# Kernel tuning notes

Measured on AMD Instinct MI355X. Metric: run time of the kernel, lower is better.

The kernel has to match this reference:

```python
import jax, jax.numpy as jnp
import numpy as np

B, C, N = 16, 4, 100
S = 96            # args.seq_len
L = 2 * S         # time-domain length
F = S + 1         # rfft bins == module's self.seq_len
D = 128           # d_model
M = 16            # delay components
H = 8             # num_heads (hard-coded)
HD = D // H       # head_dim
P = S             # pred_len


def clin(x, wr, wi, br, bi):
    # complex Linear: y = x @ W^T + b
    w = jax.lax.complex(wr, wi)
    b = jax.lax.complex(br, bi)
    return x @ w.T + b


def crelu(z):
    return jax.lax.complex(jax.nn.relu(z.real), jax.nn.relu(z.imag))


def mha(q, kv, wq, bq, wk, bk, wv, bv, wo, bo):
    # q: [B,C,N,D], kv: [B,C,N,M,D]
    Bq, Cq, Nq, Dq = q.shape
    Mq = kv.shape[3]
    Q = (q @ wq.T + bq).reshape(Bq, Cq, Nq, H, HD).transpose(0, 1, 3, 2, 4)          # [B,C,H,N,HD]
    K = (kv @ wk.T + bk).reshape(Bq, Cq, Nq, Mq, H, HD).transpose(0, 1, 4, 2, 3, 5)  # [B,C,H,N,M,HD]
    V = (kv @ wv.T + bv).reshape(Bq, Cq, Nq, Mq, H, HD).transpose(0, 1, 4, 2, 3, 5)
    K = K.reshape(Bq, Cq, H, Nq * Mq, HD)
    V = V.reshape(Bq, Cq, H, Nq * Mq, HD)
    scale = float(D) ** -0.5
    scores = jnp.einsum('bchne,bchme->bchnm', Q, K) * scale   # [B,C,H,N,N*M]
    w = jax.nn.softmax(scores, axis=-1)
    o = jnp.einsum('bchnm,bchme->bchne', w, V)                # [B,C,H,N,HD]
    o = o.transpose(0, 1, 3, 2, 4).reshape(Bq, Cq, Nq, Dq)
    return o @ wo.T + bo


def setup_inputs() -> dict:
    key = jax.random.key(0)
    ks = jax.random.split(key, 48)
    i = iter(range(48))
    def n(shape, s=0.05):
        return jax.random.normal(ks[next(i)], shape, jnp.float32) * s
    inp = {}
    inp['xp'] = jax.random.normal(ks[next(i)], (B, C, N, L), jnp.float32)
    inp['freq_weights'] = jnp.ones((F,), jnp.float32)
    inp['temp_real'] = n((M, F), 0.02)
    inp['temp_imag'] = n((M, F), 0.02)
    # complex Linears (real/imag weight & bias)
    inp['fc1_wr'] = n((D, F)); inp['fc1_wi'] = n((D, F)); inp['fc1_br'] = jnp.zeros((D,), jnp.float32); inp['fc1_bi'] = jnp.zeros((D,), jnp.float32)
    inp['fc2_wr'] = n((D, D)); inp['fc2_wi'] = n((D, D)); inp['fc2_br'] = jnp.zeros((D,), jnp.float32); inp['fc2_bi'] = jnp.zeros((D,), jnp.float32)
    inp['fc3_wr'] = n((F, D)); inp['fc3_wi'] = n((F, D)); inp['fc3_br'] = jnp.zeros((F,), jnp.float32); inp['fc3_bi'] = jnp.zeros((F,), jnp.float32)
    inp['fc4_wr'] = n((D, F)); inp['fc4_wi'] = n((D, F)); inp['fc4_br'] = jnp.zeros((D,), jnp.float32); inp['fc4_bi'] = jnp.zeros((D,), jnp.float32)
    inp['fc5_wr'] = n((D, D)); inp['fc5_wi'] = n((D, D)); inp['fc5_br'] = jnp.zeros((D,), jnp.float32); inp['fc5_bi'] = jnp.zeros((D,), jnp.float32)
    for pfx in ('ra', 'ia'):
        for nm in ('wq', 'wk', 'wv', 'wo'):
            inp[f'{pfx}_{nm}'] = n((D, D))
            inp[f'{pfx}_b{nm[1]}'] = n((D,), 0.01)
    inp['op1_w'] = n((4 * P, 2 * P)); inp['op1_b'] = jnp.zeros((4 * P,), jnp.float32)
    inp['op2_w'] = n((P, 4 * P)); inp['op2_b'] = jnp.zeros((P,), jnp.float32)
    return inp


def reference(xp, freq_weights, temp_real, temp_imag,
              fc1_wr, fc1_wi, fc1_br, fc1_bi,
              fc2_wr, fc2_wi, fc2_br, fc2_bi,
              fc3_wr, fc3_wi, fc3_br, fc3_bi,
              fc4_wr, fc4_wi, fc4_br, fc4_bi,
              fc5_wr, fc5_wi, fc5_br, fc5_bi,
              ra_wq, ra_bq, ra_wk, ra_bk, ra_wv, ra_bv, ra_wo, ra_bo,
              ia_wq, ia_bq, ia_wk, ia_bk, ia_wv, ia_bv, ia_wo, ia_bo,
              op1_w, op1_b, op2_w, op2_b):
    xf = jnp.fft.rfft(xp, axis=-1)                       # [B,C,N,F] complex64
    xf = xf * jax.nn.sigmoid(freq_weights)
    temp = jax.lax.complex(temp_real, temp_imag)          # [M,F]
    xt = xf[..., None, :] * temp                          # [B,C,N,M,F]
    e = crelu(clin(xt, fc1_wr, fc1_wi, fc1_br, fc1_bi))
    e = clin(e, fc2_wr, fc2_wi, fc2_br, fc2_bi)           # [B,C,N,M,D]
    g = crelu(clin(xf, fc4_wr, fc4_wi, fc4_br, fc4_bi))
    g = clin(g, fc5_wr, fc5_wi, fc5_br, fc5_bi)           # [B,C,N,D]
    o_r = mha(g.real, e.real, ra_wq, ra_bq, ra_wk, ra_bk, ra_wv, ra_bv, ra_wo, ra_bo) + g.real
    o_i = mha(g.imag, e.imag, ia_wq, ia_bq, ia_wk, ia_bk, ia_wv, ia_bv, ia_wo, ia_bo) + g.imag
    o = jax.lax.complex(o_r, o_i)
    o = clin(o, fc3_wr, fc3_wi, fc3_br, fc3_bi)           # [B,C,N,F]
    ot = jnp.fft.irfft(o, n=L, axis=-1)                   # [B,C,N,L] float32
    of = ot.reshape(-1, 2 * P)
    h = jax.nn.relu(of @ op1_w.T + op1_b)
    out = (h @ op2_w.T + op2_b).reshape(B, C, N, P)
    return out
```

## Files before the change

kernel.cpp:

```cpp
#include <hip/hip_runtime.h>
#include <hip/hip_bf16.h>

#define NB 16
#define NC 4
#define NN 100
#define NL 192
#define NF 97
#define ND 128
#define NM 16
#define NH 8
#define NHD 16
#define NP 96
#define NR (NB*NC*NN)
#define NBC (NB*NC)
#define KP1 224

typedef __bf16 bf16x8 __attribute__((ext_vector_type(8)));
typedef float f32x4 __attribute__((ext_vector_type(4)));
typedef float f32x16 __attribute__((ext_vector_type(16)));
typedef short s16x8 __attribute__((ext_vector_type(8)));
typedef short s16x4 __attribute__((ext_vector_type(4)));
typedef float f32x4v __attribute__((ext_vector_type(4)));

__device__ __forceinline__ float bf2f(unsigned short u){
  union { unsigned int i; float f; } x; x.i = ((unsigned int)u) << 16; return x.f;
}
__device__ __forceinline__ unsigned short f2bf(float v){
  __hip_bfloat16 h = __float2bfloat16(v);
  return *reinterpret_cast<unsigned short*>(&h);
}
__device__ __forceinline__ float fexp2(float x){
  float r; asm("v_exp_f32 %0, %1\n\ts_nop 0" : "=v"(r) : "v"(x)); return r;
}

__global__ void k_prep(const float* __restrict__ fw,
                       const float* __restrict__ fc1_wr, const float* __restrict__ fc1_wi,
                       const float* __restrict__ tr_, const float* __restrict__ ti_,
                       const float* __restrict__ fc4_wr, const float* __restrict__ fc4_wi,
                       const float* __restrict__ op1_w, const float* __restrict__ op2_w,
                       const float* __restrict__ xp,
                       unsigned short* __restrict__ Tt, unsigned short* __restrict__ Wbig,
                       unsigned short* __restrict__ Wg1,
                       unsigned short* __restrict__ Wop1, unsigned short* __restrict__ Wop2,
                       unsigned short* __restrict__ Xpb, unsigned short* __restrict__ Xpbf){
  int b = blockIdx.x, c = threadIdx.x;
  if (b < 256){
    if (c >= KP1) return;
    int l = b;
    float v = 0.f;
    if (l < NL && c < 2*NF){
      int f = (c < NF) ? c : c - NF;
      float s = 1.f/(1.f+expf(-fw[f]));
      int ph = (f*l) % NL;
      float ang = (float)ph * (6.283185307179586f/(float)NL);
      float sv, cv; sincosf(ang, &sv, &cv);
      v = (c < NF) ? s*cv : -s*sv;
    }
    Tt[(size_t)l*KP1 + c] = f2bf(v);
  } else if (b < 256+4096){
    if (c >= KP1) return;
    int nIdx = b - 256;
    int m = nIdx >> 8, p = (nIdx >> 7) & 1, d = nIdx & 127;
    float v = 0.f;
    if (c < 2*NF){
      int f = (c < NF) ? c : c - NF;
      float tr = tr_[m*NF+f], ti = ti_[m*NF+f];
      float wr_ = fc1_wr[d*NF+f], wi_ = fc1_wi[d*NF+f];
      float w1r = tr*wr_ - ti*wi_;
      float w1i = tr*wi_ + ti*wr_;
      if (p == 0) v = (c < NF) ? w1r : -w1i;
      else        v = (c < NF) ? w1i :  w1r;
    }
    Wbig[(size_t)nIdx*KP1 + c] = f2bf(v);
  } else if (b < 256+4096+256){
    if (c >= KP1) return;
    int n = b - (256+4096);
    int p = n >> 7, d = n & 127;
    float v = 0.f;
    if (c < NF) v = p ? fc4_wi[d*NF+c] : fc4_wr[d*NF+c];
    else if (c < 2*NF){
      int f = c - NF;
      v = p ? fc4_wr[d*NF+f] : -fc4_wi[d*NF+f];
    }
    Wg1[(size_t)n*KP1 + c] = f2bf(v);
  } else if (b < 4608+480){
    int i = (b-4608)*256 + c;
    const int N1 = 384*NL;
    if (i < N1){ Wop1[i] = f2bf(op1_w[i]); return; }
    int j = i - N1;
    if (j < 128*384){
      int n = j / 384, t2 = j - n*384;
      Wop2[j] = f2bf((n < NP) ? op2_w[n*384 + t2] : 0.f);
    }
  } else {
    size_t i = ((size_t)(b-5088)*256 + c)*8;
    f32x4v a = *(const f32x4v*)(xp + i);
    f32x4v bb = *(const f32x4v*)(xp + i + 4);
    s16x8 o;
#pragma unroll
    for (int e=0;e<4;e++){ o[e] = (short)f2bf(a[e]); o[4+e] = (short)f2bf(bb[e]); }
    *(s16x8*)(Xpb + i) = o;
    int row = (int)(i / NL);
    int colg = (int)(i % NL) >> 3;
    int rb = row >> 4, rl = row & 15;
    int ch = colg >> 2, cg = colg & 3;
    int lane = rl + (cg << 4);
    *(s16x8*)(Xpbf + ((((size_t)rb*6 + ch)*64 + lane)*8)) = o;
  }
}

__global__ void k_prep2(const float* __restrict__ fc2_wr, const float* __restrict__ fc2_wi,
                        const float* __restrict__ fc2_br, const float* __restrict__ fc2_bi,
                        const float* __restrict__ ra_wk, const float* __restrict__ ra_bk,
                        const float* __restrict__ ra_wv, const float* __restrict__ ra_bv,
                        const float* __restrict__ ia_wk, const float* __restrict__ ia_bk,
                        const float* __restrict__ ia_wv, const float* __restrict__ ia_bv,
                        const float* __restrict__ fc5_wr, const float* __restrict__ fc5_wi,
                        const float* __restrict__ fc5_br, const float* __restrict__ fc5_bi,
                        const float* __restrict__ ra_wq, const float* __restrict__ ra_bq,
                        const float* __restrict__ ia_wq, const float* __restrict__ ia_bq,
                        const float* __restrict__ fc3_wr, const float* __restrict__ fc3_wi,
                        const float* __restrict__ fc3_br, const float* __restrict__ fc3_bi,
                        unsigned short* __restrict__ comb2f, float* __restrict__ cbias,
                        unsigned short* __restrict__ Wg2, float* __restrict__ bg2,
                        float* __restrict__ A_, float* __restrict__ B_, float* __restrict__ c0_){
  __shared__ float icL[NF], isL[NF];
  int b = blockIdx.x, t = threadIdx.x;
  if (b < 1032){
    if (t >= 128) return;
    int k = b >> 3, c = b & 7, d = t;
    if (k == ND){
      if (c >= 4) return;
      const float* w = ra_wk; const float* bb = ra_bk; const float* fb = fc2_br;
      switch(c){
        case 0: w=ra_wk; bb=ra_bk; fb=fc2_br; break;
        case 1: w=ra_wv; bb=ra_bv; fb=fc2_br; break;
        case 2: w=ia_wk; bb=ia_bk; fb=fc2_bi; break;
        case 3: w=ia_wv; bb=ia_bv; fb=fc2_bi; break;
      }
      float s = bb[d];
      for (int j=0;j<ND;j++) s += w[d*ND+j]*fb[j];
      cbias[c*ND+d] = s;
      return;
    }
    const float* w = ra_wk; const float* f2 = fc2_wr; float sign = 1.f;
    switch(c){
      case 0: w=ra_wk; f2=fc2_wr; sign= 1.f; break;
      case 1: w=ra_wk; f2=fc2_wi; sign=-1.f; break;
      case 2: w=ra_wv; f2=fc2_wr; sign= 1.f; break;
      case 3: w=ra_wv; f2=fc2_wi; sign=-1.f; break;
      case 4: w=ia_wk; f2=fc2_wi; sign= 1.f; break;
      case 5: w=ia_wk; f2=fc2_wr; sign= 1.f; break;
      case 6: w=ia_wv; f2=fc2_wi; sign= 1.f; break;
      case 7: w=ia_wv; f2=fc2_wr; sign= 1.f; break;
    }
    float s = 0.f;
    for (int j=0;j<ND;j++) s += w[d*ND+j]*f2[j*ND+k];
    int cOut = c >> 1, p = c & 1;
    int jj = d >> 4, rl = d & 15;
    int col = p*ND + k;
    int ch = col >> 5, cg = (col >> 3) & 3, e = col & 7;
    int lane = rl + (cg << 4);
    comb2f[((((size_t)(cOut*8 + ch))*8 + jj)*64 + lane)*8 + e] = f2bf(sign*s);
  } else if (b < 1032+512){
    int q = b - 1032, c = t;
    int k = c & 127; bool ti = (c >= 128);
    const float SCL = 0.08838834764831845f * 1.4426950408889634f;
    float v = 0.f;
    if (q < 128){
      const float* f5 = ti ? fc5_wi : fc5_wr; float sg = ti ? -1.f : 1.f;
      float s = 0.f;
      for (int j=0;j<ND;j++) s += ra_wq[q*ND+j]*f5[j*ND+k];
      v = sg*s*SCL;
    } else if (q < 256){
      int qq = q-128;
      const float* f5 = ti ? fc5_wr : fc5_wi;
      float s = 0.f;
      for (int j=0;j<ND;j++) s += ia_wq[qq*ND+j]*f5[j*ND+k];
      v = s*SCL;
    } else if (q < 384){
      int d = q-256;
      v = ti ? -fc5_wi[d*ND+k] : fc5_wr[d*ND+k];
    } else {
      int d = q-384;
      v = ti ? fc5_wr[d*ND+k] : fc5_wi[d*ND+k];
    }
    Wg2[(size_t)q*256 + c] = f2bf(v);
    if (c == 0){
      float bb;
      if (q < 128){ bb = ra_bq[q]; for (int j=0;j<ND;j++) bb += ra_wq[q*ND+j]*fc5_br[j]; bb *= SCL; }
      else if (q < 256){ int qq=q-128; bb = ia_bq[qq]; for (int j=0;j<ND;j++) bb += ia_wq[qq*ND+j]*fc5_bi[j]; bb *= SCL; }
      else if (q < 384) bb = fc5_br[q-256];
      else bb = fc5_bi[q-384];
      bg2[q] = bb;
    }
  } else {
    int l = b - 1544, d = t;
    if (d < NF){
      float w = ((d==0)||(d==NF-1)) ? 1.f : 2.f;
      w *= (1.f/(float)NL);
      int ph = (d*l) % NL;
      float ang = (float)ph * (6.283185307179586f/(float)NL);
      float sv, cv; sincosf(ang, &sv, &cv);
      icL[d] = w*cv; isL[d] = w*sv;
    }
    __syncthreads();
    if (d < 128){
      float a = 0.f, bb = 0.f;
      for (int f=0;f<NF;f++){
        float ic = icL[f], is = isL[f];
        float wr = fc3_wr[f*ND+d], wi = fc3_wi[f*ND+d];
        a += ic*wr - is*wi;
        bb -= ic*wi + is*wr;
      }
      A_[l*ND+d] = a; B_[l*ND+d] = bb;
      if (d == 0){
        float cc = 0.f;
        for (int f=0;f<NF;f++) cc += icL[f]*fc3_br[f] - isL[f]*fc3_bi[f];
        c0_[l] = cc;
      }
    }
  }
}

__global__ void k_wt1(const float* __restrict__ A_, const float* __restrict__ B_,
                      const float* __restrict__ c0_,
                      const float* __restrict__ ra_wo, const float* __restrict__ ra_bo,
                      const float* __restrict__ ia_wo, const float* __restrict__ ia_bo,
                      unsigned short* __restrict__ WT1, float* __restrict__ bT1){
  int l = blockIdx.x;
  int c = threadIdx.x;
  float v = 0.f;
  if (l < NL){
    if (c < 128) v = A_[l*ND+c];
    else if (c < 256) v = B_[l*ND+(c-128)];
    else if (c < 384){
      int k = c-256; float s = 0.f;
      for (int j=0;j<ND;j++) s += A_[l*ND+j]*ra_wo[j*ND+k];
      v = s;
    } else {
      int k = c-384; float s = 0.f;
      for (int j=0;j<ND;j++) s += B_[l*ND+j]*ia_wo[j*ND+k];
      v = s;
    }
  }
  WT1[(size_t)l*512 + c] = f2bf(v);
  if (c == 0){
    float bb = 0.f;
    if (l < NL){
      bb = c0_[l];
      for (int j=0;j<ND;j++) bb += A_[l*ND+j]*ra_bo[j] + B_[l*ND+j]*ia_bo[j];
    }
    bT1[l] = bb;
  }
}

template<int MT, int KT, int MODE>
__global__ __launch_bounds__(256) void k_gemm(
    const unsigned short* __restrict__ A, int lda,
    const unsigned short* __restrict__ Bw,
    const float* __restrict__ b0, const float* __restrict__ b1,
    void* __restrict__ Cv, int ldc)
{
  constexpr int NI = MT/32;
  __shared__ unsigned short As[MT][40];
  __shared__ unsigned short Bs[128][40];
  int t = threadIdx.x;
  int bm = blockIdx.x, bn = blockIdx.y;
  int w = t >> 6, l = t & 63;
  int wm = w >> 1, wn = w & 1;
  f32x4 acc[NI][4] = {};
  int r0 = t >> 2, c0 = (t & 3) * 8;
  const unsigned short* Ag = A + (size_t)(bm*MT)*lda;
  const unsigned short* Bg = Bw + (size_t)(bn*128)*KT;
  int lr = l & 15, lk = (l >> 4) * 8;
  for (int k0 = 0; k0 < KT; k0 += 32){
    s16x8 a0 = *(const s16x8*)(Ag + (size_t)r0*lda + k0 + c0);
    s16x8 a1;
    if constexpr (MT == 128) a1 = *(const s16x8*)(Ag + (size_t)(r0+64)*lda + k0 + c0);
    s16x8 bv0 = *(const s16x8*)(Bg + (size_t)r0*KT + k0 + c0);
    s16x8 bv1 = *(const s16x8*)(Bg + (size_t)(r0+64)*KT + k0 + c0);
    __syncthreads();
    *(s16x8*)(&As[r0][c0]) = a0;
    if constexpr (MT == 128) *(s16x8*)(&As[r0+64][c0]) = a1;
    *(s16x8*)(&Bs[r0][c0]) = bv0;
    *(s16x8*)(&Bs[r0+64][c0]) = bv1;
    __syncthreads();
    bf16x8 af[NI], bfr[4];
#pragma unroll
    for (int i=0;i<NI;i++) af[i]  = *(const bf16x8*)(&As[wm*(MT/2) + i*16 + lr][lk]);
#pragma unroll
    for (int j=0;j<4;j++) bfr[j] = *(const bf16x8*)(&Bs[wn*64 + j*16 + lr][lk]);
#pragma unroll
    for (int i=0;i<NI;i++)
#pragma unroll
      for (int j=0;j<4;j++)
        acc[i][j] = __builtin_amdgcn_mfma_f32_16x16x32_bf16(af[i], bfr[j], acc[i][j], 0, 0, 0);
  }
  int lr4 = (l >> 4) * 4, lc = l & 15;
#pragma unroll
  for (int i=0;i<NI;i++){
#pragma unroll
    for (int j=0;j<4;j++){
      int n = bn*128 + wn*64 + j*16 + lc;
      float bias;
      if constexpr (MODE == 1) bias = ((n>>7)&1) ? b1[n&127] : b0[n&127];
      else if constexpr (MODE == 4) bias = (n < NP) ? b0[n] : 0.f;
      else if constexpr (MODE == 6 || MODE == 7) bias = 0.f;
      else bias = b0[n];
#pragma unroll
      for (int q=0;q<4;q++){
        int row = bm*MT + wm*(MT/2) + i*16 + lr4 + q;
        float v = acc[i][j][q] + bias;
        if constexpr (MODE == 1 || MODE == 3) v = fmaxf(v, 0.f);
        if constexpr (MODE == 4){
          if (n < NP) ((float*)Cv)[(size_t)row*ldc + n] = v;
        } else if constexpr (MODE == 6){
          if (n < NL) ((unsigned short*)Cv)[(size_t)row*ldc + n] = f2bf(v);
        } else if constexpr (MODE == 7){
          if (n < NL){
            int m2 = row >> 8, rt = row & 255;
            int jj = rt >> 4, rl2 = rt & 15;
            int ch = n >> 5, cg = (n >> 3) & 3, e = n & 7;
            int lane = rl2 + (cg << 4);
            ((unsigned short*)Cv)[((((size_t)(m2*6 + ch))*16 + jj)*64 + lane)*8 + e] = f2bf(v);
          }
        } else {
          ((unsigned short*)Cv)[(size_t)row*ldc + n] = f2bf(v);
        }
      }
    }
  }
}

__global__ __launch_bounds__(256, 4) void k_fuse(
    const unsigned short* __restrict__ Xpbf,
    const unsigned short* __restrict__ Wbig2f,
    const float* __restrict__ fc1_br, const float* __restrict__ fc1_bi,
    const unsigned short* __restrict__ comb2f,
    const float* __restrict__ cbias,
    unsigned short* __restrict__ Kg,
    unsigned short* __restrict__ Vt)
{
  __shared__ unsigned short act2f[8][4][64][8];
  int t = threadIdx.x;
  int bm = blockIdx.x, m = blockIdx.y;
  int w = t >> 6, l = t & 63;
  int lc = l & 15, lr4 = (l >> 4) * 4;
  int rbase = bm*64;

  f32x4 acc1[4][4] = {};
  const unsigned short* Af = Xpbf + ((size_t)(bm*4)*6)*512;
  const unsigned short* Bf = Wbig2f + ((size_t)m*6)*16*512;
#pragma unroll 2
  for (int ch = 0; ch < 6; ch++){
    bf16x8 af[4], bfj[4];
#pragma unroll
    for (int i=0;i<4;i++)
      af[i] = *(const bf16x8*)(Af + ((size_t)i*6 + ch)*512 + l*8);
#pragma unroll
    for (int j=0;j<4;j++)
      bfj[j] = *(const bf16x8*)(Bf + ((size_t)ch*16 + w*4 + j)*512 + l*8);
#pragma unroll
    for (int i=0;i<4;i++)
#pragma unroll
      for (int j=0;j<4;j++)
        acc1[i][j] = __builtin_amdgcn_mfma_f32_16x16x32_bf16(af[i], bfj[j], acc1[i][j], 0, 0, 0);
  }
#pragma unroll
  for (int i=0;i<4;i++){
#pragma unroll
    for (int j=0;j<4;j++){
      int col = w*64 + j*16 + lc;
      float bias = ((col>>7)&1) ? fc1_bi[col&127] : fc1_br[col&127];
      int ch = col >> 5, cg = (col >> 3) & 3, e = col & 7;
#pragma unroll
      for (int q=0;q<4;q++)
        act2f[ch][i][(lr4 + q) + (cg << 4)][e] = f2bf(fmaxf(acc1[i][j][q] + bias, 0.f));
    }
  }
  __syncthreads();

  for (int bn2 = 0; bn2 < 4; bn2++){
    const unsigned short* Cf = comb2f + ((size_t)bn2*8)*8*512;
    int call = bn2 >> 1, isV = bn2 & 1;
    if (!isV){
      f32x4 accS[2][4] = {};
#pragma unroll 4
      for (int ch = 0; ch < 8; ch++){
        bf16x8 af[4], bfr[2];
#pragma unroll
        for (int i=0;i<4;i++)
          af[i] = *(const bf16x8*)(&act2f[ch][i][l][0]);
#pragma unroll
        for (int j=0;j<2;j++)
          bfr[j] = *(const bf16x8*)(Cf + ((size_t)ch*8 + w*2 + j)*512 + l*8);
#pragma unroll
        for (int j=0;j<2;j++)
#pragma unroll
          for (int i=0;i<4;i++)
            accS[j][i] = __builtin_amdgcn_mfma_f32_16x16x32_bf16(bfr[j], af[i], accS[j][i], 0, 0, 0);
      }
#pragma unroll
      for (int j=0;j<2;j++){
        int n2q = w*32 + j*16 + lr4;
        f32x4v cb4 = *(const f32x4v*)(cbias + bn2*128 + n2q);
        int h = n2q >> 4, d0 = n2q & 15;
#pragma unroll
        for (int i=0;i<4;i++){
          int rr = rbase + i*16 + lc;
          int bc = rr/100, n = rr - bc*100;
          int kk = m*100 + n;
          s16x4 v4;
#pragma unroll
          for (int q=0;q<4;q++) v4[q] = (short)f2bf(accS[j][i][q] + cb4[q]);
          *(s16x4*)(Kg + ((((size_t)(call*NBC + bc))*8 + h)*1600 + kk)*16 + d0) = v4;
        }
      }
    } else {
      f32x4 acc[4][2] = {};
#pragma unroll 4
      for (int ch = 0; ch < 8; ch++){
        bf16x8 af[4], bfr[2];
#pragma unroll
        for (int i=0;i<4;i++)
          af[i] = *(const bf16x8*)(&act2f[ch][i][l][0]);
#pragma unroll
        for (int j=0;j<2;j++)
          bfr[j] = *(const bf16x8*)(Cf + ((size_t)ch*8 + w*2 + j)*512 + l*8);
#pragma unroll
        for (int i=0;i<4;i++)
#pragma unroll
          for (int j=0;j<2;j++)
            acc[i][j] = __builtin_amdgcn_mfma_f32_16x16x32_bf16(af[i], bfr[j], acc[i][j], 0, 0, 0);
      }
#pragma unroll
      for (int i=0;i<4;i++){
        int rr0 = rbase + i*16 + lr4;
        int bc = rr0/100, n = rr0 - bc*100;
        int kk = m*100 + n;
#pragma unroll
        for (int j=0;j<2;j++){
          int n2 = w*32 + j*16 + lc;
          float bias = cbias[bn2*128 + n2];
          s16x4 v4;
#pragma unroll
          for (int q=0;q<4;q++) v4[q] = (short)f2bf(acc[i][j][q] + bias);
          *(s16x4*)(Vt + ((size_t)(call*NBC + bc)*128 + n2)*1600 + kk) = v4;
        }
      }
    }
  }
}

__global__ __launch_bounds__(256, 4) void k_attn3(
    const unsigned short* __restrict__ BIG,
    const unsigned short* __restrict__ Kg,
    const unsigned short* __restrict__ Vt,
    unsigned short* __restrict__ BIGo)
{
  int h = blockIdx.x, bc = blockIdx.y, call = blockIdx.z;
  int t = threadIdx.x;
  int wv = t >> 6, l = t & 63;
  int lane31 = l & 31, hi = l >> 5;
  int qoff = call*128, ooff = 512 + call*128;
  __shared__ float xch[4][32];

  const unsigned short* Kh = Kg + (((size_t)(call*NBC + bc))*8 + h)*1600*16;
  const unsigned short* Vh = Vt + ((((size_t)(call*NBC + bc))*8 + h)*16)*1600;

  int qrow = wv*32 + lane31;
  bf16x8 qf = {};
  if (qrow < NN)
    qf = *(const bf16x8*)(BIG + (size_t)(bc*NN + qrow)*768 + qoff + h*NHD + hi*8);

  f32x16 acc = {};
  float m = -1e30f, lsum = 0.f;
  const f32x16 zero16 = {};
  int vd = lane31 & 15;

  auto tile = [&](bf16x8 kf0, bf16x8 kf1, int cc0){
    bf16x8 vfr[4];
#pragma unroll
    for (int ks=0; ks<4; ks++)
      vfr[ks] = *(const bf16x8*)(Vh + (size_t)vd*1600 + cc0 + ks*16 + hi*8);

    __builtin_amdgcn_s_setprio(1);
    f32x16 s0 = __builtin_amdgcn_mfma_f32_32x32x16_bf16(kf0, qf, zero16, 0, 0, 0);
    f32x16 s1 = __builtin_amdgcn_mfma_f32_32x32x16_bf16(kf1, qf, zero16, 0, 0, 0);
    __builtin_amdgcn_s_setprio(0);
    float p[32];
#pragma unroll
    for (int r2=0;r2<16;r2++){ p[r2] = s0[r2]; p[16+r2] = s1[r2]; }

    float t8[8];
#pragma unroll
    for (int r2=0;r2<8;r2++)
      t8[r2] = fmaxf(fmaxf(p[r2], p[r2+8]), fmaxf(p[r2+16], p[r2+24]));
#pragma unroll
    for (int r2=0;r2<4;r2++) t8[r2] = fmaxf(t8[r2], t8[r2+4]);
    float pm = fmaxf(fmaxf(t8[0], t8[1]), fmaxf(t8[2], t8[3]));
    pm = fmaxf(pm, __shfl_xor(pm, 32));

    if (__any(pm > m + 8.f)){
      float M = fmaxf(m, pm);
      float alpha = fexp2(m - M);
      lsum *= alpha;
      if (l < 32) xch[wv][l] = alpha;
#pragma unroll
      for (int r2=0;r2<16;r2++)
        acc[r2] *= xch[wv][(r2&3) + 8*(r2>>2) + 4*hi];
      m = M;
    }
#pragma unroll
    for (int r2=0;r2<32;r2++) p[r2] = fexp2(p[r2] - m);
    float s8[8];
#pragma unroll
    for (int r2=0;r2<8;r2++) s8[r2] = (p[r2] + p[r2+8]) + (p[r2+16] + p[r2+24]);
#pragma unroll
    for (int r2=0;r2<4;r2++) s8[r2] += s8[r2+4];
    lsum += (s8[0]+s8[1]) + (s8[2]+s8[3]);

#pragma unroll
    for (int ks=0; ks<4; ks++){
      unsigned int a, b, c, dd, sa, sb, sc2, sd;
      asm("v_cvt_pk_bf16_f32 %0, %1, %2" : "=v"(a)  : "v"(p[8*ks+0]), "v"(p[8*ks+1]));
      asm("v_cvt_pk_bf16_f32 %0, %1, %2" : "=v"(b)  : "v"(p[8*ks+4]), "v"(p[8*ks+5]));
      asm("v_cvt_pk_bf16_f32 %0, %1, %2" : "=v"(c)  : "v"(p[8*ks+2]), "v"(p[8*ks+3]));
      asm("v_cvt_pk_bf16_f32 %0, %1, %2" : "=v"(dd) : "v"(p[8*ks+6]), "v"(p[8*ks+7]));
      sa = __shfl_xor(a, 32); sb = __shfl_xor(b, 32);
      sc2 = __shfl_xor(c, 32); sd = __shfl_xor(dd, 32);
      union { unsigned int u[4]; bf16x8 v; } pu;
      pu.u[0] = hi ? sb : a;
      pu.u[1] = hi ? sd : c;
      pu.u[2] = hi ? b  : sa;
      pu.u[3] = hi ? dd : sc2;
      acc = __builtin_amdgcn_mfma_f32_32x32x16_bf16(pu.v, vfr[ks], acc, 0, 0, 0);
    }
  };

  bf16x8 k0a = *(const bf16x8*)(Kh + (size_t)lane31*16 + hi*8);
  bf16x8 k1a = *(const bf16x8*)(Kh + (size_t)(32 + lane31)*16 + hi*8);
  bf16x8 k0b, k1b;
#pragma unroll 1
  for (int cc0 = 0; cc0 < NN*NM; cc0 += 128){
    if (cc0 + 64 < NN*NM){
      k0b = *(const bf16x8*)(Kh + (size_t)(cc0 + 64 + lane31)*16 + hi*8);
      k1b = *(const bf16x8*)(Kh + (size_t)(cc0 + 96 + lane31)*16 + hi*8);
    }
    tile(k0a, k1a, cc0);
    if (cc0 + 64 >= NN*NM) break;
    if (cc0 + 128 < NN*NM){
      k0a = *(const bf16x8*)(Kh + (size_t)(cc0 + 128 + lane31)*16 + hi*8);
      k1a = *(const bf16x8*)(Kh + (size_t)(cc0 + 160 + lane31)*16 + hi*8);
    }
    tile(k0b, k1b, cc0 + 64);
  }

  lsum += __shfl_xor(lsum, 32);
  float inv = 1.f / lsum;
  if (l < 32) xch[wv][l] = inv;
  if (lane31 < 16){
    int d = lane31;
#pragma unroll
    for (int r2=0;r2<16;r2++){
      int q = (r2&3) + 8*(r2>>2) + 4*hi;
      int qr2 = wv*32 + q;
      if (qr2 < NN){
        float iv = xch[wv][q];
        BIGo[(size_t)(bc*NN + qr2)*768 + ooff + h*NHD + d] = f2bf(acc[r2]*iv);
      }
    }
  }
}

extern "C" void kernel_launch(void* const* d_in, const int* in_sizes, int n_in,
                              void* d_out, int out_size, void* d_ws, size_t ws_size,
                              hipStream_t stream){
  const float* xp     = (const float*)d_in[0];
  const float* fw     = (const float*)d_in[1];
  const float* temp_r = (const float*)d_in[2];
  const float* temp_i = (const float*)d_in[3];
  const float* fc1_wr=(const float*)d_in[4],  *fc1_wi=(const float*)d_in[5],
             *fc1_br=(const float*)d_in[6],  *fc1_bi=(const float*)d_in[7];
  const float* fc2_wr=(const float*)d_in[8],  *fc2_wi=(const float*)d_in[9],
             *fc2_br=(const float*)d_in[10], *fc2_bi=(const float*)d_in[11];
  const float* fc3_wr=(const float*)d_in[12], *fc3_wi=(const float*)d_in[13],
             *fc3_br=(const float*)d_in[14], *fc3_bi=(const float*)d_in[15];
  const float* fc4_wr=(const float*)d_in[16], *fc4_wi=(const float*)d_in[17],
             *fc4_br=(const float*)d_in[18], *fc4_bi=(const float*)d_in[19];
  const float* fc5_wr=(const float*)d_in[20], *fc5_wi=(const float*)d_in[21],
             *fc5_br=(const float*)d_in[22], *fc5_bi=(const float*)d_in[23];
  const float* ra_wq=(const float*)d_in[24], *ra_bq=(const float*)d_in[25],
             *ra_wk=(const float*)d_in[26], *ra_bk=(const float*)d_in[27],
             *ra_wv=(const float*)d_in[28], *ra_bv=(const float*)d_in[29],
             *ra_wo=(const float*)d_in[30], *ra_bo=(const float*)d_in[31];
  const float* ia_wq=(const float*)d_in[32], *ia_bq=(const float*)d_in[33],
             *ia_wk=(const float*)d_in[34], *ia_bk=(const float*)d_in[35],
             *ia_wv=(const float*)d_in[36], *ia_bv=(const float*)d_in[37],
             *ia_wo=(const float*)d_in[38], *ia_bo=(const float*)d_in[39];
  const float* op1_w=(const float*)d_in[40], *op1_b=(const float*)d_in[41],
             *op2_w=(const float*)d_in[42], *op2_b=(const float*)d_in[43];
  float* out = (float*)d_out;

  char* ws = (char*)d_ws;
  size_t off = 0;
  auto alloc = [&](size_t bytes)->char*{
    char* p = ws + off;
    off += (bytes + 255) & ~(size_t)255;
    return p;
  };
  unsigned short* Tt     = (unsigned short*)alloc((size_t)256*KP1*2);
  unsigned short* Wbig   = (unsigned short*)alloc((size_t)4096*KP1*2);
  unsigned short* Wbig2f = (unsigned short*)alloc((size_t)4096*NL*2);
  unsigned short* comb2f = (unsigned short*)alloc((size_t)512*256*2);
  float* cbias= (float*)alloc((size_t)4*ND*4);
  unsigned short* Wg1    = (unsigned short*)alloc((size_t)256*KP1*2);
  unsigned short* Wg1f   = (unsigned short*)alloc((size_t)256*NL*2);
  unsigned short* Wg2    = (unsigned short*)alloc((size_t)512*256*2);
  float* bg2  = (float*)alloc((size_t)512*4);
  float* A_   = (float*)alloc((size_t)NL*ND*4);
  float* B_   = (float*)alloc((size_t)NL*ND*4);
  float* c0_  = (float*)alloc((size_t)NL*4);
  unsigned short* WT1    = (unsigned short*)alloc((size_t)256*512*2);
  float* bT1  = (float*)alloc((size_t)256*4);
  unsigned short* Wop1   = (unsigned short*)alloc((size_t)384*NL*2);
  unsigned short* Wop2   = (unsigned short*)alloc((size_t)128*384*2);
  unsigned short* Xpb    = (unsigned short*)alloc((size_t)NR*NL*2);
  unsigned short* Xpbf   = (unsigned short*)alloc((size_t)NR*NL*2);
  unsigned short* actg   = (unsigned short*)alloc((size_t)NR*256*2);
  unsigned short* Kg     = (unsigned short*)alloc((size_t)2*NBC*NH*1600*16*2);
  unsigned short* Vt     = (unsigned short*)alloc((size_t)2*NBC*NH*16*1600*2);
  unsigned short* BIG    = (unsigned short*)alloc((size_t)NR*768*2);
  unsigned short* C1     = (unsigned short*)alloc((size_t)NR*256*2);
  unsigned short* hbuf   = (unsigned short*)alloc((size_t)NR*384*2);

  k_prep<<<5688, 256, 0, stream>>>(fw, fc1_wr, fc1_wi, temp_r, temp_i,
                                   fc4_wr, fc4_wi, op1_w, op2_w, xp,
                                   Tt, Wbig, Wg1, Wop1, Wop2, Xpb, Xpbf);
  k_prep2<<<1736, 256, 0, stream>>>(fc2_wr, fc2_wi, fc2_br, fc2_bi,
                                    ra_wk, ra_bk, ra_wv, ra_bv,
                                    ia_wk, ia_bk, ia_wv, ia_bv,
                                    fc5_wr, fc5_wi, fc5_br, fc5_bi,
                                    ra_wq, ra_bq, ia_wq, ia_bq,
                                    fc3_wr, fc3_wi, fc3_br, fc3_bi,
                                    comb2f, cbias, Wg2, bg2, A_, B_, c0_);
  k_wt1<<<256, 512, 0, stream>>>(A_, B_, c0_, ra_wo, ra_bo, ia_wo, ia_bo, WT1, bT1);
  k_gemm<128,KP1,7><<<dim3(32, 2), 256, 0, stream>>>(Wbig, KP1, Tt, nullptr, nullptr, Wbig2f, NL);
  k_gemm<128,KP1,6><<<dim3(2, 2), 256, 0, stream>>>(Wg1, KP1, Tt, nullptr, nullptr, Wg1f, NL);

  k_gemm<64,NL,1><<<dim3(100, 2), 256, 0, stream>>>(Xpb, NL, Wg1f, fc4_br, fc4_bi, actg, 256);
  k_gemm<64,256,2><<<dim3(100, 4), 256, 0, stream>>>(actg, 256, Wg2, bg2, nullptr, BIG, 768);
  k_fuse<<<dim3(100, NM), 256, 0, stream>>>(Xpbf, Wbig2f, fc1_br, fc1_bi, comb2f, cbias, Kg, Vt);
  k_attn3<<<dim3(NH, NBC, 2), 256, 0, stream>>>(BIG, Kg, Vt, BIG);
  k_gemm<64,512,2><<<dim3(100, 2), 256, 0, stream>>>(BIG+256, 768, WT1, bT1, nullptr, C1, 256);
  k_gemm<64,192,3><<<dim3(100, 3), 256, 0, stream>>>(C1, 256, Wop1, op1_b, nullptr, hbuf, 384);
  k_gemm<64,384,4><<<dim3(100, 1), 256, 0, stream>>>(hbuf, 384, Wop2, op2_b, nullptr, out, NP);
}
```

Before: 199.3 us.

## Split attention key range in two with a separate log-sum-exp combine kernel

The attention kernel now splits the 1600 keys into two halves across an extra grid dimension, doubling the number of blocks from 1024 to 2048. Each half writes unnormalized fp32 partial outputs plus its running max and sum. A new combine kernel merges the halves and writes bf16 into the big activation buffer. The goal is better CU occupancy on the attention stage, paid for with an extra launch, partial-result traffic, and the loss of the double-buffered K prefetch.

Result: slower. 207.1 us (+4.0%).

```diff
diff --git a/kernel.cpp b/kernel.cpp
--- a/kernel.cpp
+++ b/kernel.cpp
@@ -457,13 +457,15 @@
     const unsigned short* __restrict__ BIG,
     const unsigned short* __restrict__ Kg,
     const unsigned short* __restrict__ Vt,
-    unsigned short* __restrict__ BIGo)
+    float* __restrict__ Opart,
+    float* __restrict__ MLp)
 {
-  int h = blockIdx.x, bc = blockIdx.y, call = blockIdx.z;
+  int h = blockIdx.x, bc = blockIdx.y, z = blockIdx.z;
+  int call = z >> 1, half = z & 1;
   int t = threadIdx.x;
   int wv = t >> 6, l = t & 63;
   int lane31 = l & 31, hi = l >> 5;
-  int qoff = call*128, ooff = 512 + call*128;
+  int qoff = call*128;
   __shared__ float xch[4][32];
 
   const unsigned short* Kh = Kg + (((size_t)(call*NBC + bc))*8 + h)*1600*16;
@@ -479,7 +481,13 @@
   const f32x16 zero16 = {};
   int vd = lane31 & 15;
 
-  auto tile = [&](bf16x8 kf0, bf16x8 kf1, int cc0){
+  const int t0 = half ? 768 : 0;
+  const int t1 = half ? NN*NM : 768;
+
+#pragma unroll 1
+  for (int cc0 = t0; cc0 < t1; cc0 += 64){
+    bf16x8 kf0 = *(const bf16x8*)(Kh + (size_t)(cc0 + lane31)*16 + hi*8);
+    bf16x8 kf1 = *(const bf16x8*)(Kh + (size_t)(cc0 + 32 + lane31)*16 + hi*8);
     bf16x8 vfr[4];
 #pragma unroll
     for (int ks=0; ks<4; ks++)
@@ -537,41 +545,43 @@
       pu.u[3] = hi ? dd : sc2;
       acc = __builtin_amdgcn_mfma_f32_32x32x16_bf16(pu.v, vfr[ks], acc, 0, 0, 0);
     }
-  };
-
-  bf16x8 k0a = *(const bf16x8*)(Kh + (size_t)lane31*16 + hi*8);
-  bf16x8 k1a = *(const bf16x8*)(Kh + (size_t)(32 + lane31)*16 + hi*8);
-  bf16x8 k0b, k1b;
-#pragma unroll 1
-  for (int cc0 = 0; cc0 < NN*NM; cc0 += 128){
-    if (cc0 + 64 < NN*NM){
-      k0b = *(const bf16x8*)(Kh + (size_t)(cc0 + 64 + lane31)*16 + hi*8);
-      k1b = *(const bf16x8*)(Kh + (size_t)(cc0 + 96 + lane31)*16 + hi*8);
-    }
-    tile(k0a, k1a, cc0);
-    if (cc0 + 64 >= NN*NM) break;
-    if (cc0 + 128 < NN*NM){
-      k0a = *(const bf16x8*)(Kh + (size_t)(cc0 + 128 + lane31)*16 + hi*8);
-      k1a = *(const bf16x8*)(Kh + (size_t)(cc0 + 160 + lane31)*16 + hi*8);
-    }
-    tile(k0b, k1b, cc0 + 64);
   }
 
   lsum += __shfl_xor(lsum, 32);
-  float inv = 1.f / lsum;
-  if (l < 32) xch[wv][l] = inv;
+  size_t pb = ((size_t)z*NBC + bc)*NH + h;
+  if (l < 32){
+    int qr = wv*32 + l;
+    if (qr < NN){
+      MLp[(pb*NN + qr)*2 + 0] = m;
+      MLp[(pb*NN + qr)*2 + 1] = lsum;
+    }
+  }
   if (lane31 < 16){
     int d = lane31;
 #pragma unroll
     for (int r2=0;r2<16;r2++){
       int q = (r2&3) + 8*(r2>>2) + 4*hi;
       int qr2 = wv*32 + q;
-      if (qr2 < NN){
-        float iv = xch[wv][q];
-        BIGo[(size_t)(bc*NN + qr2)*768 + ooff + h*NHD + d] = f2bf(acc[r2]*iv);
-      }
-    }
-  }
+      if (qr2 < NN)
+        Opart[(pb*NN + qr2)*16 + d] = acc[r2];
+    }
+  }
+}
+
+__global__ void k_comb(const float* __restrict__ Opart, const float* __restrict__ MLp,
+                       unsigned short* __restrict__ BIGo){
+  int q = blockIdx.x, bc = blockIdx.y, call = blockIdx.z;
+  int t = threadIdx.x;
+  int h = t >> 4, d = t & 15;
+  size_t pb0 = ((size_t)(call*2+0)*NBC + bc)*NH + h;
+  size_t pb1 = ((size_t)(call*2+1)*NBC + bc)*NH + h;
+  float m0 = MLp[(pb0*NN + q)*2], l0 = MLp[(pb0*NN + q)*2 + 1];
+  float m1 = MLp[(pb1*NN + q)*2], l1 = MLp[(pb1*NN + q)*2 + 1];
+  float M = fmaxf(m0, m1);
+  float a0 = fexp2(m0 - M), a1 = fexp2(m1 - M);
+  float L = a0*l0 + a1*l1;
+  float v = (a0*Opart[(pb0*NN + q)*16 + d] + a1*Opart[(pb1*NN + q)*16 + d]) / L;
+  BIGo[(size_t)(bc*NN + q)*768 + 512 + call*128 + h*16 + d] = f2bf(v);
 }
 
 extern "C" void kernel_launch(void* const* d_in, const int* in_sizes, int n_in,
@@ -634,6 +644,8 @@
   unsigned short* BIG    = (unsigned short*)alloc((size_t)NR*768*2);
   unsigned short* C1     = (unsigned short*)alloc((size_t)NR*256*2);
   unsigned short* hbuf   = (unsigned short*)alloc((size_t)NR*384*2);
+  float* Opart = (float*)alloc((size_t)4*NBC*NH*NN*16*4);
+  float* MLp   = (float*)alloc((size_t)4*NBC*NH*NN*2*4);
 
   k_prep<<<5688, 256, 0, stream>>>(fw, fc1_wr, fc1_wi, temp_r, temp_i,
                                    fc4_wr, fc4_wi, op1_w, op2_w, xp,
@@ -652,7 +664,8 @@
   k_gemm<64,NL,1><<<dim3(100, 2), 256, 0, stream>>>(Xpb, NL, Wg1f, fc4_br, fc4_bi, actg, 256);
   k_gemm<64,256,2><<<dim3(100, 4), 256, 0, stream>>>(actg, 256, Wg2, bg2, nullptr, BIG, 768);
   k_fuse<<<dim3(100, NM), 256, 0, stream>>>(Xpbf, Wbig2f, fc1_br, fc1_bi, comb2f, cbias, Kg, Vt);
-  k_attn3<<<dim3(NH, NBC, 2), 256, 0, stream>>>(BIG, Kg, Vt, BIG);
+  k_attn3<<<dim3(NH, NBC, 4), 256, 0, stream>>>(BIG, Kg, Vt, Opart, MLp);
+  k_comb<<<dim3(NN, NBC, 2), 128, 0, stream>>>(Opart, MLp, BIG);
   k_gemm<64,512,2><<<dim3(100, 2), 256, 0, stream>>>(BIG+256, 768, WT1, bT1, nullptr, C1, 256);
   k_gemm<64,192,3><<<dim3(100, 3), 256, 0, stream>>>(C1, 256, Wop1, op1_b, nullptr, hbuf, 384);
   k_gemm<64,384,4><<<dim3(100, 1), 256, 0, stream>>>(hbuf, 384, Wop2, op2_b, nullptr, out, NP);
```

## Permute V column layout to drop cross-lane shuffles in attention PV step

Applied to the files above, without the earlier changes.

The V-projection epilogue now writes the key index in a permuted order, swapping bits 2 and 3 of the index within each 16-block. This lets the attention kernel feed the converted softmax probabilities directly as the MFMA A operand without the xor-32 lane shuffles and selects. The explicit double-buffered K prefetch loop is also replaced by a simple loop that loads K each iteration. This reduces cross-lane traffic and VALU work, but relies on the compiler to hide K load latency.

After: 198.3 us. Within noise of the previous version (-0.5%).

```diff
diff --git a/kernel.cpp b/kernel.cpp
--- a/kernel.cpp
+++ b/kernel.cpp
@@ -439,6 +439,7 @@
         int rr0 = rbase + i*16 + lr4;
         int bc = rr0/100, n = rr0 - bc*100;
         int kk = m*100 + n;
+        int kkp = (kk & ~15) | ((kk & 4) << 1) | ((kk & 8) >> 1);
 #pragma unroll
         for (int j=0;j<2;j++){
           int n2 = w*32 + j*16 + lc;
@@ -446,7 +447,7 @@
           s16x4 v4;
 #pragma unroll
           for (int q=0;q<4;q++) v4[q] = (short)f2bf(acc[i][j][q] + bias);
-          *(s16x4*)(Vt + ((size_t)(call*NBC + bc)*128 + n2)*1600 + kk) = v4;
+          *(s16x4*)(Vt + ((size_t)(call*NBC + bc)*128 + n2)*1600 + kkp) = v4;
         }
       }
     }
@@ -479,7 +480,9 @@
   const f32x16 zero16 = {};
   int vd = lane31 & 15;
 
-  auto tile = [&](bf16x8 kf0, bf16x8 kf1, int cc0){
+  for (int cc0 = 0; cc0 < NN*NM; cc0 += 64){
+    bf16x8 kf0 = *(const bf16x8*)(Kh + (size_t)(cc0 + lane31)*16 + hi*8);
+    bf16x8 kf1 = *(const bf16x8*)(Kh + (size_t)(cc0 + 32 + lane31)*16 + hi*8);
     bf16x8 vfr[4];
 #pragma unroll
     for (int ks=0; ks<4; ks++)
@@ -523,38 +526,13 @@
 
 #pragma unroll
     for (int ks=0; ks<4; ks++){
-      unsigned int a, b, c, dd, sa, sb, sc2, sd;
-      asm("v_cvt_pk_bf16_f32 %0, %1, %2" : "=v"(a)  : "v"(p[8*ks+0]), "v"(p[8*ks+1]));
-      asm("v_cvt_pk_bf16_f32 %0, %1, %2" : "=v"(b)  : "v"(p[8*ks+4]), "v"(p[8*ks+5]));
-      asm("v_cvt_pk_bf16_f32 %0, %1, %2" : "=v"(c)  : "v"(p[8*ks+2]), "v"(p[8*ks+3]));
-      asm("v_cvt_pk_bf16_f32 %0, %1, %2" : "=v"(dd) : "v"(p[8*ks+6]), "v"(p[8*ks+7]));
-      sa = __shfl_xor(a, 32); sb = __shfl_xor(b, 32);
-      sc2 = __shfl_xor(c, 32); sd = __shfl_xor(dd, 32);
       union { unsigned int u[4]; bf16x8 v; } pu;
-      pu.u[0] = hi ? sb : a;
-      pu.u[1] = hi ? sd : c;
-      pu.u[2] = hi ? b  : sa;
-      pu.u[3] = hi ? dd : sc2;
+      asm("v_cvt_pk_bf16_f32 %0, %1, %2" : "=v"(pu.u[0]) : "v"(p[8*ks+0]), "v"(p[8*ks+1]));
+      asm("v_cvt_pk_bf16_f32 %0, %1, %2" : "=v"(pu.u[1]) : "v"(p[8*ks+2]), "v"(p[8*ks+3]));
+      asm("v_cvt_pk_bf16_f32 %0, %1, %2" : "=v"(pu.u[2]) : "v"(p[8*ks+4]), "v"(p[8*ks+5]));
+      asm("v_cvt_pk_bf16_f32 %0, %1, %2" : "=v"(pu.u[3]) : "v"(p[8*ks+6]), "v"(p[8*ks+7]));
       acc = __builtin_amdgcn_mfma_f32_32x32x16_bf16(pu.v, vfr[ks], acc, 0, 0, 0);
     }
-  };
-
-  bf16x8 k0a = *(const bf16x8*)(Kh + (size_t)lane31*16 + hi*8);
-  bf16x8 k1a = *(const bf16x8*)(Kh + (size_t)(32 + lane31)*16 + hi*8);
-  bf16x8 k0b, k1b;
-#pragma unroll 1
-  for (int cc0 = 0; cc0 < NN*NM; cc0 += 128){
-    if (cc0 + 64 < NN*NM){
-      k0b = *(const bf16x8*)(Kh + (size_t)(cc0 + 64 + lane31)*16 + hi*8);
-      k1b = *(const bf16x8*)(Kh + (size_t)(cc0 + 96 + lane31)*16 + hi*8);
-    }
-    tile(k0a, k1a, cc0);
-    if (cc0 + 64 >= NN*NM) break;
-    if (cc0 + 128 < NN*NM){
-      k0a = *(const bf16x8*)(Kh + (size_t)(cc0 + 128 + lane31)*16 + hi*8);
-      k1a = *(const bf16x8*)(Kh + (size_t)(cc0 + 160 + lane31)*16 + hi*8);
-    }
-    tile(k0b, k1b, cc0 + 64);
   }
 
   lsum += __shfl_xor(lsum, 32);
```
